# Performance work log

Measured on AMD Instinct MI355X. Metric: run time of the kernel, lower is better.

Reference implementation:

```python
import jax, jax.numpy as jnp
import numpy as np

DIM = 64
HID = 64      # hidden_dim
BATCH = 16384


def setup_inputs() -> dict:
    key = jax.random.key(0)
    ks = jax.random.split(key, 11)
    s = 0.05
    x = jax.random.normal(ks[0], (BATCH, DIM), dtype=jnp.float32)
    # network 0: Linear(1,H) -> ReLU -> Linear(H,2)
    w0 = jax.random.normal(ks[1], (1, HID), dtype=jnp.float32) * s
    b0 = jax.random.normal(ks[2], (HID,), dtype=jnp.float32) * s
    v0 = jax.random.normal(ks[3], (HID, 2), dtype=jnp.float32) * s
    c0 = jax.random.normal(ks[4], (2,), dtype=jnp.float32) * s
    # networks 1..DIM-1: Linear(i,H) -> ReLU -> Linear(H,H) -> ReLU -> Linear(H,2)
    # first-layer weights padded to full width DIM; columns >= i are masked out in reference().
    W1 = jax.random.normal(ks[5], (DIM - 1, DIM, HID), dtype=jnp.float32) * s
    B1 = jax.random.normal(ks[6], (DIM - 1, HID), dtype=jnp.float32) * s
    W2 = jax.random.normal(ks[7], (DIM - 1, HID, HID), dtype=jnp.float32) * s
    B2 = jax.random.normal(ks[8], (DIM - 1, HID), dtype=jnp.float32) * s
    W3 = jax.random.normal(ks[9], (DIM - 1, HID, 2), dtype=jnp.float32) * s
    B3 = jax.random.normal(ks[10], (DIM - 1, 2), dtype=jnp.float32) * s
    return {"x": x, "w0": w0, "b0": b0, "v0": v0, "c0": c0,
            "W1": W1, "B1": B1, "W2": W2, "B2": B2, "W3": W3, "B3": B3}


def reference(x, w0, b0, v0, c0, W1, B1, W2, B2, W3, B3):
    B, dim = x.shape
    # mask[i, j] = 1 if j < (i+1): network i+1 sees x[:, :i+1] prefix of width i+1... actually width i+1? No:
    # network index k (k = 1..dim-1) sees x[:, :k]. Row i of the stacks corresponds to k = i+1,
    # so valid input columns are j < i+1.
    mask = (jnp.arange(dim)[None, :] <= jnpp_dummy) if False else (jnp.arange(dim)[None, :] < (jnp.arange(1, dim)[:, None]))
    mask = mask.astype(x.dtype)                      # [dim-1, dim]
    W1m = W1 * mask[:, :, None]                      # zero out padded input columns
    h1 = jax.nn.relu(jnp.einsum('bd,idh->bih', x, W1m) + B1)   # [B, dim-1, H]
    h2 = jax.nn.relu(jnp.einsum('bih,ihg->big', h1, W2) + B2)  # [B, dim-1, H]
    out = jnp.einsum('big,igo->bio', h2, W3) + B3               # [B, dim-1, 2]
    # network 0 receives a constant ones input -> output is constant across the batch
    h0 = jax.nn.relu(w0[0] + b0)                     # [H]
    out0 = h0 @ v0 + c0                              # [2]
    out0 = jnp.broadcast_to(out0[None, None, :], (B, 1, 2))
    full = jnp.concatenate([out0, out], axis=1)      # [B, dim, 2]
    scales = jnp.clip(full[..., 0], -5.0, 5.0)
    translations = full[..., 1]
    return scales, translations

jnp_dummy = None
```

## Files before the change

kernel.cpp:

```cpp
#include <hip/hip_runtime.h>
#include <hip/hip_bf16.h>

#define BATCH 16384

typedef __attribute__((ext_vector_type(8))) short short8;
typedef __attribute__((ext_vector_type(4))) short short4v;
typedef __attribute__((ext_vector_type(2))) short sshort2;
typedef __attribute__((ext_vector_type(8))) unsigned short ushort8;
typedef __attribute__((ext_vector_type(4))) unsigned short ushort4v;
typedef __attribute__((ext_vector_type(4))) float float4v;

#define FR_STRIDE  18944u
#define FR_SIZE    (63u * FR_STRIDE)
#define OFF_A2     8192u
#define OFF_A3     16384u
#define OFF_B1     18432u
#define OFF_B2     18688u
#define XBF_SIZE   2097152u
#define FR_ELEMS   1184

__device__ __forceinline__ unsigned int packbf2(float a, float b) {
#if __has_builtin(__builtin_amdgcn_cvt_pk_bf16_f32)
    typedef __attribute__((ext_vector_type(2))) __bf16 bf2_t;
    union { bf2_t h; unsigned int u; } v;
    v.h = __builtin_amdgcn_cvt_pk_bf16_f32(a, b);
    return v.u;
#else
    union { __hip_bfloat162 h; unsigned int u; } v;
    v.h = __float22bfloat162_rn(make_float2(a, b));
    return v.u;
#endif
}
__device__ __forceinline__ unsigned int relu_pk(unsigned int u) {
#if __has_builtin(__builtin_elementwise_max)
    union { sshort2 s; unsigned int w; } v; v.w = u;
    v.s = __builtin_elementwise_max(v.s, (sshort2)0);
    return v.w;
#else
    unsigned int lo = (u & 0x8000u) ? 0u : (u & 0xFFFFu);
    unsigned int hi = (u & 0x80000000u) ? 0u : (u & 0xFFFF0000u);
    return lo | hi;
#endif
}
__device__ __forceinline__ unsigned int cvt_relu(float a, float b) {
    return relu_pk(packbf2(a, b));
}
__device__ __forceinline__ unsigned short f2bf(float a) {
    union { __hip_bfloat16 h; unsigned short u; } v;
    v.h = __float2bfloat16(a);
    return v.u;
}

__device__ __forceinline__ void gl_lds16(const char* gsrc, char* ldst) {
    __builtin_amdgcn_global_load_lds(
        (const __attribute__((address_space(1))) unsigned int*)gsrc,
        (__attribute__((address_space(3))) unsigned int*)ldst,
        16, 0, 0);
}

__global__ __launch_bounds__(256) void setup_kernel(
    const float* __restrict__ x,
    const float* __restrict__ W1,
    const float* __restrict__ W2,
    const float* __restrict__ W3,
    const float* __restrict__ B1,
    const float* __restrict__ B2,
    char* __restrict__ frag,
    char* __restrict__ xbf)
{
    const int b = blockIdx.x;
    const int t = threadIdx.x;

    if (b >= 63) {
        const int idx = (b - 63) * 256 + t;
        const float* xp = x + (size_t)idx * 16;
        char* dst = xbf + (size_t)idx * 32;
        #pragma unroll
        for (int h = 0; h < 2; ++h) {
            float4v f0 = *(const float4v*)(xp + h * 8);
            float4v f1 = *(const float4v*)(xp + h * 8 + 4);
            union { ushort8 s; unsigned int u[4]; } p;
            p.u[0] = packbf2(f0[0], f0[1]);
            p.u[1] = packbf2(f0[2], f0[3]);
            p.u[2] = packbf2(f1[0], f1[1]);
            p.u[3] = packbf2(f1[2], f1[3]);
            *(ushort8*)(dst + h * 16) = p.s;
        }
        return;
    }

    __shared__ float sW1[4096];
    __shared__ float sW2[4096];

    const int kn   = b;
    const int net  = kn + 1;
    const int lane = t & 63;
    const int grp  = t >> 6;
    const int lq   = lane & 15;
    const int quad = lane >> 4;

    {
        const float4v* s1 = (const float4v*)(W1 + kn * 4096);
        const float4v* s2 = (const float4v*)(W2 + kn * 4096);
        #pragma unroll
        for (int i = 0; i < 4; ++i) {
            ((float4v*)sW1)[i * 256 + t] = s1[i * 256 + t];
            ((float4v*)sW2)[i * 256 + t] = s2[i * 256 + t];
        }
    }
    __syncthreads();

    char* base = frag + (size_t)kn * FR_STRIDE;

    {
        const int h = lq + 16 * grp;
        ushort8 a10, a11;
        #pragma unroll
        for (int j = 0; j < 8; ++j) {
            const int d0 = quad * 8 + j;
            const int d1 = d0 + 32;
            a10[j] = (d0 < net) ? f2bf(sW1[d0 * 64 + h]) : (unsigned short)0;
            a11[j] = (d1 < net) ? f2bf(sW1[d1 * 64 + h]) : (unsigned short)0;
        }
        char* dst = base + grp * 2048 + lane * 32;
        *(ushort8*)(dst)      = a10;
        *(ushort8*)(dst + 16) = a11;
    }

    {
        const int g = lq + 16 * grp;
        #pragma unroll
        for (int th = 0; th < 4; ++th) {
            ushort4v v;
            #pragma unroll
            for (int i = 0; i < 4; ++i) {
                const int h = quad * 4 + 16 * th + i;
                v[i] = f2bf(sW2[h * 64 + g]);
            }
            *(ushort4v*)(base + OFF_A2 + grp * 2048 + th * 512 + lane * 8) = v;
        }
    }

    {
        ushort4v v;
        #pragma unroll
        for (int i = 0; i < 4; ++i) {
            const int g = quad * 4 + 16 * grp + i;
            v[i] = (lq < 2) ? f2bf(W3[kn * 128 + g * 2 + lq]) : (unsigned short)0;
        }
        *(ushort4v*)(base + OFF_A3 + grp * 512 + lane * 8) = v;
    }

    if (t < 64) {
        *(float*)(base + OFF_B1 + t * 4) = B1[kn * 64 + t];
        *(float*)(base + OFF_B2 + t * 4) = B2[kn * 64 + t];
    }
}

template <bool XBF>
__global__ __launch_bounds__(256, 3) void arnet_main4(
    const float* __restrict__ x,
    const char* __restrict__ xbf,
    const char* __restrict__ frag,
    const float* __restrict__ w0, const float* __restrict__ b0,
    const float* __restrict__ v0, const float* __restrict__ c0,
    const float* __restrict__ B3,
    float* __restrict__ out)
{
    const int bi    = blockIdx.x;
    const int chunk = bi & 63;
    const int g     = bi >> 6;
    const int t     = threadIdx.x;

    const int lane = t & 63;
    const int w    = t >> 6;
    const int lq   = lane & 15;
    const int quad = lane >> 4;

    __shared__ __align__(16) char sFrag[2][FR_STRIDE];
    __shared__ float sOut[2][256][5];

    const int rowbase = chunk * 256 + w * 64;

    short8 xf[4][2];
    #pragma unroll
    for (int tm = 0; tm < 4; ++tm) {
        if (XBF) {
            const char* base = xbf + (size_t)(rowbase + 16 * tm + lq) * 128 + quad * 16;
            xf[tm][0] = *(const short8*)(base);
            xf[tm][1] = *(const short8*)(base + 64);
        } else {
            const float* xr = x + (size_t)(rowbase + 16 * tm + lq) * 64 + quad * 8;
            #pragma unroll
            for (int half = 0; half < 2; ++half) {
                float4v f0 = *(const float4v*)(xr + 32 * half);
                float4v f1 = *(const float4v*)(xr + 32 * half + 4);
                union { short8 s; unsigned int u[4]; } p;
                p.u[0] = packbf2(f0[0], f0[1]);
                p.u[1] = packbf2(f0[2], f0[3]);
                p.u[2] = packbf2(f1[0], f1[1]);
                p.u[3] = packbf2(f1[2], f1[3]);
                xf[tm][half] = p.s;
            }
        }
    }

    auto stage = [&](int net_, char* dstb) {
        const char* src = frag + (size_t)(net_ - 1) * FR_STRIDE;
        #pragma unroll
        for (int i = 0; i < 5; ++i) {
            const int e = i * 256 + t;
            if (e < FR_ELEMS)
                gl_lds16(src + e * 16, dstb + e * 16);
        }
    };

    const int first = (g == 0) ? 1 : 0;
    stage(g * 4 + first, sFrag[first & 1]);
    __syncthreads();

    #pragma unroll 1
    for (int idx = 0; idx < 4; ++idx) {
        const int net = g * 4 + idx;

        if (idx + 1 < 4 && idx + 1 > first)
            stage(g * 4 + idx + 1, sFrag[(idx + 1) & 1]);

        if (net == 0) {
            float s = 0.f, tr = 0.f;
            #pragma unroll 8
            for (int j = 0; j < 64; ++j) {
                float h = fmaxf(w0[j] + b0[j], 0.f);
                s  += h * v0[2 * j];
                tr += h * v0[2 * j + 1];
            }
            s += c0[0];
            tr += c0[1];
            s = fminf(fmaxf(s, -5.f), 5.f);
            sOut[0][t][0] = s;
            sOut[1][t][0] = tr;
            __syncthreads();
            continue;
        }

        const int kn = net - 1;
        const char* sf  = sFrag[idx & 1];
        const char* pA1 = sf + lane * 32;
        const char* pA2 = sf + OFF_A2 + lane * 8;
        const char* pA3 = sf + OFF_A3 + lane * 8;
        const float* bB1 = (const float*)(sf + OFF_B1);
        const float* bB2 = (const float*)(sf + OFF_B2);

        float4v acc2[4][4];
        #pragma unroll
        for (int th = 0; th < 4; ++th) {
            short8 a10 = *(const short8*)(pA1 + th * 2048);
            short8 a11 = *(const short8*)(pA1 + th * 2048 + 16);
            float4v bias1 = *(const float4v*)(bB1 + quad * 4 + 16 * th);
            short4v bf1[4];
            #pragma unroll
            for (int tm = 0; tm < 4; ++tm) {
                float4v acc1;
                acc1 = __builtin_amdgcn_mfma_f32_16x16x32_bf16(a10, xf[tm][0], bias1, 0, 0, 0);
                acc1 = __builtin_amdgcn_mfma_f32_16x16x32_bf16(a11, xf[tm][1], acc1, 0, 0, 0);
                union { short4v s; unsigned int u[2]; } pk;
                pk.u[0] = cvt_relu(acc1[0], acc1[1]);
                pk.u[1] = cvt_relu(acc1[2], acc1[3]);
                bf1[tm] = pk.s;
            }
            if (th == 0) {
                #pragma unroll
                for (int tg = 0; tg < 4; ++tg) {
                    short4v a2 = *(const short4v*)(pA2 + tg * 2048);
                    float4v bias2 = *(const float4v*)(bB2 + quad * 4 + 16 * tg);
                    #pragma unroll
                    for (int tm = 0; tm < 4; ++tm)
                        acc2[tg][tm] = __builtin_amdgcn_mfma_f32_16x16x16bf16_1k(a2, bf1[tm], bias2, 0, 0, 0);
                }
            } else {
                #pragma unroll
                for (int tg = 0; tg < 4; ++tg) {
                    short4v a2 = *(const short4v*)(pA2 + tg * 2048 + th * 512);
                    #pragma unroll
                    for (int tm = 0; tm < 4; ++tm)
                        acc2[tg][tm] = __builtin_amdgcn_mfma_f32_16x16x16bf16_1k(a2, bf1[tm], acc2[tg][tm], 0, 0, 0);
                }
            }
        }

        float4v c3v;
        c3v[0] = B3[kn * 2]; c3v[1] = B3[kn * 2 + 1]; c3v[2] = 0.f; c3v[3] = 0.f;
        float4v acc3[4];
        #pragma unroll
        for (int tg = 0; tg < 4; ++tg) {
            short4v a3 = *(const short4v*)(pA3 + tg * 512);
            #pragma unroll
            for (int tm = 0; tm < 4; ++tm) {
                union { short4v s; unsigned int u[2]; } pk;
                pk.u[0] = cvt_relu(acc2[tg][tm][0], acc2[tg][tm][1]);
                pk.u[1] = cvt_relu(acc2[tg][tm][2], acc2[tg][tm][3]);
                acc3[tm] = __builtin_amdgcn_mfma_f32_16x16x16bf16_1k(a3, pk.s, (tg == 0) ? c3v : acc3[tm], 0, 0, 0);
            }
        }

        if (quad == 0) {
            #pragma unroll
            for (int tm = 0; tm < 4; ++tm) {
                const int lr = w * 64 + 16 * tm + lq;
                sOut[0][lr][idx] = fminf(fmaxf(acc3[tm][0], -5.f), 5.f);
                sOut[1][lr][idx] = acc3[tm][1];
            }
        }
        __syncthreads();
    }

    {
        const int row = t;
        const size_t grow = (size_t)chunk * 256 + row;
        #pragma unroll
        for (int o = 0; o < 2; ++o) {
            float4v v4;
            #pragma unroll
            for (int j = 0; j < 4; ++j) v4[j] = sOut[o][row][j];
            float* dst = out + ((size_t)o * BATCH + grow) * 64 + 4 * g;
            *(float4v*)(dst) = v4;
        }
    }
}

#define WPAD 72
__global__ __launch_bounds__(256) void arnet_fallback(
    const float* __restrict__ x, const float* __restrict__ w0, const float* __restrict__ b0,
    const float* __restrict__ v0, const float* __restrict__ c0,
    const float* __restrict__ W1, const float* __restrict__ B1,
    const float* __restrict__ W2, const float* __restrict__ B2,
    const float* __restrict__ W3, const float* __restrict__ B3,
    float* __restrict__ out)
{
    const int bi = blockIdx.x;
    const int net = bi >> 5;
    const int tile = bi & 31;
    const int t = threadIdx.x;
    if (net == 0) {
        float s = 0.f, tr = 0.f;
        for (int j = 0; j < 64; ++j) {
            float h = fmaxf(w0[j] + b0[j], 0.f);
            s += h * v0[2 * j]; tr += h * v0[2 * j + 1];
        }
        s += c0[0]; tr += c0[1];
        s = fminf(fmaxf(s, -5.f), 5.f);
        const size_t r0 = (size_t)tile * 512;
        out[(r0 + t) * 64] = s; out[(size_t)BATCH * 64 + (r0 + t) * 64] = tr;
        out[(r0 + 256 + t) * 64] = s; out[(size_t)BATCH * 64 + (r0 + 256 + t) * 64] = tr;
        return;
    }
    __shared__ unsigned short sW1T[64 * WPAD];
    __shared__ unsigned short sW2T[64 * WPAD];
    __shared__ unsigned short sW3T[2 * 64];
    __shared__ float sB1[64];
    __shared__ float sB2[64];
    const int kn = net - 1;
    {
        const int hb = (t & 15) * 4, jb = (t >> 4) * 4;
        const float* src1 = W1 + kn * 4096;
        const float* src2 = W2 + kn * 4096;
        float4v a[4], b[4];
        for (int jj = 0; jj < 4; ++jj) {
            a[jj] = *(const float4v*)(src1 + (jb + jj) * 64 + hb);
            if (jb + jj >= net) a[jj] = (float4v)0.f;
            b[jj] = *(const float4v*)(src2 + (jb + jj) * 64 + hb);
        }
        for (int hh = 0; hh < 4; ++hh) {
            ushort4v ra, rb;
            for (int jj = 0; jj < 4; ++jj) { ra[jj] = f2bf(a[jj][hh]); rb[jj] = f2bf(b[jj][hh]); }
            *(ushort4v*)(&sW1T[(hb + hh) * WPAD + jb]) = ra;
            *(ushort4v*)(&sW2T[(hb + hh) * WPAD + jb]) = rb;
        }
    }
    if (t < 64) {
        sW3T[t] = f2bf(W3[kn * 128 + t * 2]);
        sW3T[64 + t] = f2bf(W3[kn * 128 + t * 2 + 1]);
        sB1[t] = B1[kn * 64 + t];
        sB2[t] = B2[kn * 64 + t];
    }
    const float b30 = B3[kn * 2], b31 = B3[kn * 2 + 1];
    __syncthreads();
    const int lane = t & 63, w = t >> 6, lq = lane & 15, quad = lane >> 4;
    for (int pass = 0; pass < 2; ++pass) {
        const int rowbase = tile * 512 + pass * 256 + w * 64;
        short8 xf[4][2];
        for (int tm = 0; tm < 4; ++tm) {
            const float* xr = x + (size_t)(rowbase + 16 * tm + lq) * 64 + quad * 8;
            for (int half = 0; half < 2; ++half) {
                float4v f0 = *(const float4v*)(xr + 32 * half);
                float4v f1 = *(const float4v*)(xr + 32 * half + 4);
                union { short8 s; unsigned int u[4]; } p;
                p.u[0] = packbf2(f0[0], f0[1]); p.u[1] = packbf2(f0[2], f0[3]);
                p.u[2] = packbf2(f1[0], f1[1]); p.u[3] = packbf2(f1[2], f1[3]);
                xf[tm][half] = p.s;
            }
        }
        float4v acc2[4][4];
        for (int tg = 0; tg < 4; ++tg) {
            float4v bias2 = *(const float4v*)(&sB2[quad * 4 + 16 * tg]);
            for (int tm = 0; tm < 4; ++tm) acc2[tg][tm] = bias2;
        }
        for (int th = 0; th < 4; ++th) {
            float4v bias1 = *(const float4v*)(&sB1[quad * 4 + 16 * th]);
            short8 a10 = *(const short8*)(&sW1T[(lq + 16 * th) * WPAD + quad * 8]);
            short8 a11 = *(const short8*)(&sW1T[(lq + 16 * th) * WPAD + quad * 8 + 32]);
            float4v acc1[4];
            for (int tm = 0; tm < 4; ++tm) {
                acc1[tm] = bias1;
                acc1[tm] = __builtin_amdgcn_mfma_f32_16x16x32_bf16(a10, xf[tm][0], acc1[tm], 0, 0, 0);
                acc1[tm] = __builtin_amdgcn_mfma_f32_16x16x32_bf16(a11, xf[tm][1], acc1[tm], 0, 0, 0);
            }
            short4v bf1[4];
            for (int tm = 0; tm < 4; ++tm) {
                union { short4v s; unsigned int u[2]; } pk;
                pk.u[0] = cvt_relu(acc1[tm][0], acc1[tm][1]);
                pk.u[1] = cvt_relu(acc1[tm][2], acc1[tm][3]);
                bf1[tm] = pk.s;
            }
            for (int tg = 0; tg < 4; ++tg) {
                short4v a2 = *(const short4v*)(&sW2T[(lq + 16 * tg) * WPAD + quad * 4 + 16 * th]);
                for (int tm = 0; tm < 4; ++tm)
                    acc2[tg][tm] = __builtin_amdgcn_mfma_f32_16x16x16bf16_1k(a2, bf1[tm], acc2[tg][tm], 0, 0, 0);
            }
        }
        float4v acc3[4];
        for (int tm = 0; tm < 4; ++tm) { acc3[tm][0] = b30; acc3[tm][1] = b31; acc3[tm][2] = 0.f; acc3[tm][3] = 0.f; }
        for (int tg = 0; tg < 4; ++tg) {
            short4v a3 = (short4v)0;
            if (lq < 2) a3 = *(const short4v*)(&sW3T[lq * 64 + quad * 4 + 16 * tg]);
            for (int tm = 0; tm < 4; ++tm) {
                union { short4v s; unsigned int u[2]; } pk;
                pk.u[0] = cvt_relu(acc2[tg][tm][0], acc2[tg][tm][1]);
                pk.u[1] = cvt_relu(acc2[tg][tm][2], acc2[tg][tm][3]);
                acc3[tm] = __builtin_amdgcn_mfma_f32_16x16x16bf16_1k(a3, pk.s, acc3[tm], 0, 0, 0);
            }
        }
        if (quad == 0) {
            for (int tm = 0; tm < 4; ++tm) {
                const size_t r = (size_t)(rowbase + 16 * tm + lq);
                out[r * 64 + net] = fminf(fmaxf(acc3[tm][0], -5.f), 5.f);
                out[(size_t)BATCH * 64 + r * 64 + net] = acc3[tm][1];
            }
        }
    }
}

extern "C" void kernel_launch(void* const* d_in, const int* in_sizes, int n_in,
                              void* d_out, int out_size, void* d_ws, size_t ws_size,
                              hipStream_t stream) {
    const float* x  = (const float*)d_in[0];
    const float* w0 = (const float*)d_in[1];
    const float* b0 = (const float*)d_in[2];
    const float* v0 = (const float*)d_in[3];
    const float* c0 = (const float*)d_in[4];
    const float* W1 = (const float*)d_in[5];
    const float* B1 = (const float*)d_in[6];
    const float* W2 = (const float*)d_in[7];
    const float* B2 = (const float*)d_in[8];
    const float* W3 = (const float*)d_in[9];
    const float* B3 = (const float*)d_in[10];
    float* out = (float*)d_out;
    char* ws = (char*)d_ws;

    const dim3 blk(256);

    if (ws_size >= FR_SIZE + XBF_SIZE) {
        char* xbf = ws + FR_SIZE;
        setup_kernel<<<dim3(63 + 256), blk, 0, stream>>>(x, W1, W2, W3, B1, B2, ws, xbf);
        arnet_main4<true><<<dim3(1024), blk, 0, stream>>>(
            x, xbf, ws, w0, b0, v0, c0, B3, out);
    } else if (ws_size >= FR_SIZE) {
        setup_kernel<<<dim3(63), blk, 0, stream>>>(x, W1, W2, W3, B1, B2, ws, nullptr);
        arnet_main4<false><<<dim3(1024), blk, 0, stream>>>(
            x, nullptr, ws, w0, b0, v0, c0, B3, out);
    } else {
        arnet_fallback<<<dim3(64 * 32), blk, 0, stream>>>(
            x, w0, b0, v0, c0, W1, B1, W2, B2, W3, B3, out);
    }
}
```

Baseline: 108.5 us.

## Use 16x16x32 bf16 MFMA for layers two and three with repacked fragments

After: 104.0 us. 4.1% less time.

```diff
diff --git a/kernel.cpp b/kernel.cpp
--- a/kernel.cpp
+++ b/kernel.cpp
@@ -130,25 +130,26 @@
     {
         const int g = lq + 16 * grp;
         #pragma unroll
-        for (int th = 0; th < 4; ++th) {
-            ushort4v v;
-            #pragma unroll
-            for (int i = 0; i < 4; ++i) {
-                const int h = quad * 4 + 16 * th + i;
-                v[i] = f2bf(sW2[h * 64 + g]);
-            }
-            *(ushort4v*)(base + OFF_A2 + grp * 2048 + th * 512 + lane * 8) = v;
-        }
-    }
-
-    {
-        ushort4v v;
-        #pragma unroll
-        for (int i = 0; i < 4; ++i) {
-            const int g = quad * 4 + 16 * grp + i;
-            v[i] = (lq < 2) ? f2bf(W3[kn * 128 + g * 2 + lq]) : (unsigned short)0;
-        }
-        *(ushort4v*)(base + OFF_A3 + grp * 512 + lane * 8) = v;
+        for (int p = 0; p < 2; ++p) {
+            ushort8 v;
+            #pragma unroll
+            for (int j = 0; j < 8; ++j) {
+                const int h = 32 * p + ((j & 4) << 2) + 4 * quad + (j & 3);
+                v[j] = f2bf(sW2[h * 64 + g]);
+            }
+            *(ushort8*)(base + OFF_A2 + p * 4096 + grp * 1024 + lane * 16) = v;
+        }
+    }
+
+    if (grp < 2) {
+        const int p = grp;
+        ushort8 v;
+        #pragma unroll
+        for (int j = 0; j < 8; ++j) {
+            const int gg = 32 * p + ((j & 4) << 2) + 4 * quad + (j & 3);
+            v[j] = (lq < 2) ? f2bf(W3[kn * 128 + gg * 2 + lq]) : (unsigned short)0;
+        }
+        *(ushort8*)(base + OFF_A3 + p * 1024 + lane * 16) = v;
     }
 
     if (t < 64) {
@@ -246,44 +247,41 @@
         const int kn = net - 1;
         const char* sf  = sFrag[idx & 1];
         const char* pA1 = sf + lane * 32;
-        const char* pA2 = sf + OFF_A2 + lane * 8;
-        const char* pA3 = sf + OFF_A3 + lane * 8;
+        const char* pA2 = sf + OFF_A2 + lane * 16;
+        const char* pA3 = sf + OFF_A3 + lane * 16;
         const float* bB1 = (const float*)(sf + OFF_B1);
         const float* bB2 = (const float*)(sf + OFF_B2);
 
         float4v acc2[4][4];
         #pragma unroll
-        for (int th = 0; th < 4; ++th) {
-            short8 a10 = *(const short8*)(pA1 + th * 2048);
-            short8 a11 = *(const short8*)(pA1 + th * 2048 + 16);
-            float4v bias1 = *(const float4v*)(bB1 + quad * 4 + 16 * th);
-            short4v bf1[4];
-            #pragma unroll
-            for (int tm = 0; tm < 4; ++tm) {
-                float4v acc1;
-                acc1 = __builtin_amdgcn_mfma_f32_16x16x32_bf16(a10, xf[tm][0], bias1, 0, 0, 0);
-                acc1 = __builtin_amdgcn_mfma_f32_16x16x32_bf16(a11, xf[tm][1], acc1, 0, 0, 0);
-                union { short4v s; unsigned int u[2]; } pk;
-                pk.u[0] = cvt_relu(acc1[0], acc1[1]);
-                pk.u[1] = cvt_relu(acc1[2], acc1[3]);
-                bf1[tm] = pk.s;
-            }
-            if (th == 0) {
+        for (int p = 0; p < 2; ++p) {
+            unsigned int pk[2][2][4];
+            #pragma unroll
+            for (int s = 0; s < 2; ++s) {
+                const int th = 2 * p + s;
+                short8 a10 = *(const short8*)(pA1 + th * 2048);
+                short8 a11 = *(const short8*)(pA1 + th * 2048 + 16);
+                float4v bias1 = *(const float4v*)(bB1 + quad * 4 + 16 * th);
                 #pragma unroll
-                for (int tg = 0; tg < 4; ++tg) {
-                    short4v a2 = *(const short4v*)(pA2 + tg * 2048);
-                    float4v bias2 = *(const float4v*)(bB2 + quad * 4 + 16 * tg);
-                    #pragma unroll
-                    for (int tm = 0; tm < 4; ++tm)
-                        acc2[tg][tm] = __builtin_amdgcn_mfma_f32_16x16x16bf16_1k(a2, bf1[tm], bias2, 0, 0, 0);
+                for (int tm = 0; tm < 4; ++tm) {
+                    float4v acc1;
+                    acc1 = __builtin_amdgcn_mfma_f32_16x16x32_bf16(a10, xf[tm][0], bias1, 0, 0, 0);
+                    acc1 = __builtin_amdgcn_mfma_f32_16x16x32_bf16(a11, xf[tm][1], acc1, 0, 0, 0);
+                    pk[s][0][tm] = cvt_relu(acc1[0], acc1[1]);
+                    pk[s][1][tm] = cvt_relu(acc1[2], acc1[3]);
                 }
-            } else {
+            }
+            #pragma unroll
+            for (int tg = 0; tg < 4; ++tg) {
+                short8 a2 = *(const short8*)(pA2 + p * 4096 + tg * 1024);
+                float4v bias2 = *(const float4v*)(bB2 + quad * 4 + 16 * tg);
                 #pragma unroll
-                for (int tg = 0; tg < 4; ++tg) {
-                    short4v a2 = *(const short4v*)(pA2 + tg * 2048 + th * 512);
-                    #pragma unroll
-                    for (int tm = 0; tm < 4; ++tm)
-                        acc2[tg][tm] = __builtin_amdgcn_mfma_f32_16x16x16bf16_1k(a2, bf1[tm], acc2[tg][tm], 0, 0, 0);
+                for (int tm = 0; tm < 4; ++tm) {
+                    union { short8 s8; unsigned int u[4]; } bb;
+                    bb.u[0] = pk[0][0][tm]; bb.u[1] = pk[0][1][tm];
+                    bb.u[2] = pk[1][0][tm]; bb.u[3] = pk[1][1][tm];
+                    acc2[tg][tm] = __builtin_amdgcn_mfma_f32_16x16x32_bf16(
+                        a2, bb.s8, (p == 0) ? bias2 : acc2[tg][tm], 0, 0, 0);
                 }
             }
         }
@@ -292,14 +290,17 @@
         c3v[0] = B3[kn * 2]; c3v[1] = B3[kn * 2 + 1]; c3v[2] = 0.f; c3v[3] = 0.f;
         float4v acc3[4];
         #pragma unroll
-        for (int tg = 0; tg < 4; ++tg) {
-            short4v a3 = *(const short4v*)(pA3 + tg * 512);
-            #pragma unroll
-            for (int tm = 0; tm < 4; ++tm) {
-                union { short4v s; unsigned int u[2]; } pk;
-                pk.u[0] = cvt_relu(acc2[tg][tm][0], acc2[tg][tm][1]);
-                pk.u[1] = cvt_relu(acc2[tg][tm][2], acc2[tg][tm][3]);
-                acc3[tm] = __builtin_amdgcn_mfma_f32_16x16x16bf16_1k(a3, pk.s, (tg == 0) ? c3v : acc3[tm], 0, 0, 0);
+        for (int p = 0; p < 2; ++p) {
+            short8 a3 = *(const short8*)(pA3 + p * 1024);
+            #pragma unroll
+            for (int tm = 0; tm < 4; ++tm) {
+                union { short8 s8; unsigned int u[4]; } bb;
+                bb.u[0] = cvt_relu(acc2[2 * p][tm][0],     acc2[2 * p][tm][1]);
+                bb.u[1] = cvt_relu(acc2[2 * p][tm][2],     acc2[2 * p][tm][3]);
+                bb.u[2] = cvt_relu(acc2[2 * p + 1][tm][0], acc2[2 * p + 1][tm][1]);
+                bb.u[3] = cvt_relu(acc2[2 * p + 1][tm][2], acc2[2 * p + 1][tm][3]);
+                acc3[tm] = __builtin_amdgcn_mfma_f32_16x16x32_bf16(
+                    a3, bb.s8, (p == 0) ? c3v : acc3[tm], 0, 0, 0);
             }
         }
 
```
